# Kernel optimization log

Measured on AMD Instinct MI355X. Metric: run time of the kernel, lower is better.

Reference implementation:

```python
import jax, jax.numpy as jnp
import numpy as np

N = 131072       # total nodes (B graphs x P nodes)
P = 4096         # nodes per graph
B = 32           # graphs in batch
E = 2097152      # edges (avg degree 16)
IN_DIM = 64
HID = 128
OUT = 16
EPS = 1e-5
SLOPE = 0.01


def _degrees(idx):
    # structural degree, clamped to min 1 (as DGL GraphConv does)
    d = jax.ops.segment_sum(jnp.ones((E,), jnp.float32), idx, num_segments=N)
    return jnp.maximum(d, 1.0)


def _graph_conv(x, W, src, dst, ew):
    # DGL GraphConv, norm='both', bias=False, with scalar edge weights:
    # h = D_out^{-1/2} x ; m_v = sum_{(u->v)} w_e h_u ; out = (D_in^{-1/2} m) W
    h = x * jax.lax.rsqrt(_degrees(src))[:, None]
    m = jax.ops.segment_sum(ew[:, None] * h[src], dst, num_segments=N)  # [N, F]
    return (m * jax.lax.rsqrt(_degrees(dst))[:, None]) @ W


def _graph_norm(x, gamma, beta, alpha):
    # GraphNorm (Cai et al. / PyG, batch=None): stats over all nodes per feature
    mu = jnp.mean(x, axis=0)
    c = x - alpha * mu
    var = jnp.mean(c * c, axis=0)
    return c * jax.lax.rsqrt(var + EPS) * gamma + beta


def _mean_nodes(h, gid):
    # per-graph mean readout; every graph has exactly P nodes
    return jax.ops.segment_sum(h, gid, num_segments=B) / P


def setup_inputs() -> dict:
    key = jax.random.key(0)
    ks = jax.random.split(key, 8)
    src = jax.random.randint(ks[0], (E,), 0, N, dtype=jnp.int32)
    # keep edges within each 4096-node graph block (batched DGL graph)
    dst = (src // P) * P + jax.random.randint(ks[1], (E,), 0, P, dtype=jnp.int32)
    features = jax.random.normal(ks[2], (N, IN_DIM), jnp.float32)
    edge_weights = jax.random.uniform(ks[3], (E,), jnp.float32)
    # kaiming/xavier-scale init approximations
    W1 = jax.random.normal(ks[4], (IN_DIM, HID), jnp.float32) * np.sqrt(2.0 / IN_DIM)
    W2 = jax.random.normal(ks[5], (HID, HID), jnp.float32) * np.sqrt(2.0 / HID)
    Wc = jax.random.normal(ks[6], (OUT, 2 * HID), jnp.float32) * np.sqrt(1.0 / (2 * HID))
    ones = jnp.ones((HID,), jnp.float32)
    zeros = jnp.zeros((HID,), jnp.float32)
    return {
        'features': features, 'edge_weights': edge_weights, 'src': src, 'dst': dst,
        'W1': W1, 'W2': W2, 'Wc': Wc,
        'gamma1': ones, 'beta1': zeros, 'alpha1': ones,
        'gamma2': ones, 'beta2': zeros, 'alpha2': ones,
    }


def reference(features, edge_weights, src, dst, W1, W2, Wc,
              gamma1, beta1, alpha1, gamma2, beta2, alpha2):
    gid = jnp.arange(N, dtype=jnp.int32) // P  # node -> graph id
    h1 = _graph_conv(features, W1, src, dst, edge_weights)
    h1 = jax.nn.leaky_relu(_graph_norm(h1, gamma1, beta1, alpha1), SLOPE)
    r1 = _mean_nodes(h1, gid)                  # [B, HID]
    h2 = _graph_conv(h1, W2, src, dst, edge_weights)
    h2 = jax.nn.leaky_relu(_graph_norm(h2, gamma2, beta2, alpha2), SLOPE)
    r2 = _mean_nodes(h2, gid)                  # [B, HID]
    readouts = jnp.concatenate([r1, r2], axis=1)  # [B, 2*HID]
    return readouts @ Wc.T                     # [B, OUT]
```

## Files before the change

kernel.cpp:

```cpp
#include <hip/hip_runtime.h>
#include <hip/hip_fp16.h>

constexpr int NN   = 131072;
constexpr int PP   = 4096;
constexpr int BG   = 32;
constexpr int EE   = 2097152;
constexpr int IND  = 64;
constexpr int HH   = 128;
constexpr int CAP  = 81920;
constexpr float EPSV   = 1e-5f;
constexpr float SLOPEV = 0.01f;

typedef short bf16x8 __attribute__((ext_vector_type(8)));
typedef float f32x4  __attribute__((ext_vector_type(4)));

__device__ __forceinline__ unsigned f2bf(float f) {
    unsigned u = __float_as_uint(f);
    return (u + 0x7FFFu + ((u >> 16) & 1u)) >> 16;
}
__device__ __forceinline__ unsigned pack2bf(float lo, float hi) {
    return f2bf(lo) | (f2bf(hi) << 16);
}
__device__ __forceinline__ float bflo(unsigned p) { return __uint_as_float(p << 16); }
__device__ __forceinline__ float bfhi(unsigned p) { return __uint_as_float(p & 0xFFFF0000u); }
__device__ __forceinline__ float w16(unsigned r) {
    return __half2float(__ushort_as_half((unsigned short)(r >> 16)));
}

template <int K>
__device__ __forceinline__ void packw_body(const float* __restrict__ W,
                                           unsigned short* __restrict__ pw, int t) {
    if (t >= K * 16) return;
    int lane = t & 63, nt = (t >> 6) & 7, kt = t >> 9;
    int kbase = kt * 32 + ((lane >> 4) & 3) * 8;
    int col   = nt * 16 + (lane & 15);
    for (int j = 0; j < 8; j++)
        pw[t * 8 + j] = (unsigned short)f2bf(W[(kbase + j) * HH + col]);
}

__global__ __launch_bounds__(256) void k_prep(const float* __restrict__ features,
                                              unsigned* __restrict__ fx,
                                              const float* __restrict__ W1,
                                              unsigned short* __restrict__ pw1,
                                              const float* __restrict__ W2,
                                              unsigned short* __restrict__ pw2,
                                              int* __restrict__ gcur,
                                              float* __restrict__ racc,
                                              unsigned* __restrict__ csr2) {
    int b = blockIdx.x, t = threadIdx.x;
    if (b < 16384) {
        int i = b * 256 + t;
        float2 v = ((const float2*)features)[i];
        fx[i] = pack2bf(v.x, v.y);
        return;
    }
    if (b == 16384) {
        if (t < BG) gcur[t * 16] = t * CAP;
        for (int i = t; i < 2 * BG * HH; i += 256) racc[i] = 0.f;
        return;
    }
    if (b < 16389) { packw_body<64>(W1, pw1, (b - 16385) * 256 + t); return; }
    if (b < 16397) { packw_body<128>(W2, pw2, (b - 16389) * 256 + t); return; }
    ((uint4*)csr2)[(b - 16397) * 256 + t] = make_uint4(0, 0, 0, 0);
}

__global__ __launch_bounds__(256) void k_part(const int* __restrict__ src,
                                              const int* __restrict__ dst,
                                              const float* __restrict__ ew,
                                              int* __restrict__ gcur,
                                              uint2* __restrict__ recs) {
    __shared__ int cnt[32];
    __shared__ int start[32];
    __shared__ int gbase[32];
    __shared__ uint2 stage[4096];
    int t = threadIdx.x;
    int ebase = blockIdx.x * 4096;
    if (t < 32) cnt[t] = 0;
    __syncthreads();
    int es[16]; int ed[16]; float ev[16];
#pragma unroll
    for (int k = 0; k < 16; k++) {
        int e = ebase + k * 256 + t;
        es[k] = src[e]; ed[k] = dst[e]; ev[k] = ew[e];
        atomicAdd(&cnt[es[k] >> 12], 1);
    }
    __syncthreads();
    if (t == 0) {
        int run = 0;
        for (int g = 0; g < 32; g++) { start[g] = run; run += cnt[g]; }
    }
    __syncthreads();
    if (t < 32) {
        gbase[t] = atomicAdd(&gcur[t * 16], cnt[t]);
        cnt[t] = start[t];
    }
    __syncthreads();
#pragma unroll
    for (int k = 0; k < 16; k++) {
        int g = es[k] >> 12;
        int pos = atomicAdd(&cnt[g], 1);
        stage[pos] = make_uint2((unsigned)(es[k] & 4095) | ((unsigned)(ed[k] & 4095) << 12) |
                                ((unsigned)g << 24), __float_as_uint(ev[k]));
    }
    __syncthreads();
    for (int i = t; i < 4096; i += 256) {
        uint2 r = stage[i];
        int g = r.x >> 24;
        recs[gbase[g] + (i - start[g])] = r;
    }
}

__global__ __launch_bounds__(1024) void k_hist(const uint2* __restrict__ recs,
                                               const int* __restrict__ gcur,
                                               int* __restrict__ shist,
                                               int* __restrict__ dhist) {
    __shared__ int hs[4096];
    __shared__ int hd[4096];
    int t = threadIdx.x;
    int g = blockIdx.x >> 3, c = blockIdx.x & 7;
    int n = gcur[g * 16] - g * CAP;
    int lo = (n * c) >> 3, hi = (n * (c + 1)) >> 3;
    ((int4*)hs)[t] = make_int4(0, 0, 0, 0);
    ((int4*)hd)[t] = make_int4(0, 0, 0, 0);
    __syncthreads();
    const uint2* base = recs + (size_t)g * CAP;
    for (int i = lo + t; i < hi; i += 1024) {
        unsigned x = base[i].x;
        atomicAdd(&hs[x & 4095], 1);
        atomicAdd(&hd[(x >> 12) & 4095], 1);
    }
    __syncthreads();
    ((int4*)(shist + (size_t)blockIdx.x * 4096))[t] = ((int4*)hs)[t];
    ((int4*)(dhist + (size_t)blockIdx.x * 4096))[t] = ((int4*)hd)[t];
}

__global__ __launch_bounds__(1024) void k_offs(int* __restrict__ shist,
                                               int* __restrict__ dhist,
                                               float* __restrict__ rs_s,
                                               float* __restrict__ rsd,
                                               int* __restrict__ degd,
                                               int* __restrict__ offs) {
    __shared__ int partial[1024];
    int t = threadIdx.x, g = blockIdx.x;
    int sdeg[4] = {0, 0, 0, 0}, ddeg[4] = {0, 0, 0, 0};
#pragma unroll
    for (int c = 0; c < 8; c++) {
        int4 sv = ((const int4*)(shist + (size_t)(g * 8 + c) * 4096))[t];
        int4 dv = ((const int4*)(dhist + (size_t)(g * 8 + c) * 4096))[t];
        sdeg[0] += sv.x; sdeg[1] += sv.y; sdeg[2] += sv.z; sdeg[3] += sv.w;
        ddeg[0] += dv.x; ddeg[1] += dv.y; ddeg[2] += dv.z; ddeg[3] += dv.w;
    }
    int pdeg[4];
#pragma unroll
    for (int j = 0; j < 4; j++) {
        int idx = t * 4 + j;
        int vs = sdeg[j]; if (vs < 1) vs = 1;
        rs_s[g * PP + idx] = rsqrtf((float)vs);
        int vd = ddeg[j]; if (vd < 1) vd = 1;
        rsd[g * PP + idx]  = rsqrtf((float)vd);
        pdeg[j] = (ddeg[j] + 3) & ~3;
        degd[g * PP + idx] = pdeg[j];
    }
    partial[t] = pdeg[0] + pdeg[1] + pdeg[2] + pdeg[3];
    __syncthreads();
    for (int off = 1; off < 1024; off <<= 1) {
        int v = partial[t];
        int add = (t >= off) ? partial[t - off] : 0;
        __syncthreads();
        partial[t] = v + add;
        __syncthreads();
    }
    int run = (t == 0) ? 0 : partial[t - 1];
#pragma unroll
    for (int j = 0; j < 4; j++) {
        int idx = t * 4 + j;
        offs[g * PP + idx] = g * CAP + run;
        int nb = run;
        for (int c = 0; c < 8; c++) {
            size_t hidx = (size_t)(g * 8 + c) * 4096 + idx;
            int v = dhist[hidx];
            dhist[hidx] = nb;
            nb += v;
        }
        run += pdeg[j];
    }
}

__global__ __launch_bounds__(1024) void k_place(const uint2* __restrict__ recs,
                                                const int* __restrict__ gcur,
                                                const int* __restrict__ dhist,
                                                const float* __restrict__ rs_s,
                                                unsigned* __restrict__ csr2) {
    __shared__ int cur[4096];
    __shared__ float rss[4096];
    int t = threadIdx.x;
    int g = blockIdx.x >> 3, c = blockIdx.x & 7;
    int n = gcur[g * 16] - g * CAP;
    int lo = (n * c) >> 3, hi = (n * (c + 1)) >> 3;
    ((int4*)cur)[t] = ((const int4*)(dhist + (size_t)blockIdx.x * 4096))[t];
    ((float4*)rss)[t] = ((const float4*)(rs_s + (size_t)g * PP))[t];
    __syncthreads();
    const uint2* base = recs + (size_t)g * CAP;
    unsigned* cbase = csr2 + (size_t)g * CAP;
    for (int i = lo + t; i < hi; i += 1024) {
        uint2 r = base[i];
        int sl = r.x & 4095, dl = (r.x >> 12) & 4095;
        int pos = atomicAdd(&cur[dl], 1);
        float wf = __uint_as_float(r.y) * rss[sl];
        cbase[pos] = (unsigned)sl | ((unsigned)__half_as_ushort(__float2half(wf)) << 16);
    }
}

__global__ __launch_bounds__(256) void k_aggemm1(const unsigned* __restrict__ fx,
                                                 const unsigned* __restrict__ csr2,
                                                 const int* __restrict__ offs,
                                                 const int* __restrict__ degd,
                                                 const float* __restrict__ rsd,
                                                 const short* __restrict__ PW,
                                                 unsigned short* __restrict__ C,
                                                 float* __restrict__ part) {
    constexpr int WP = 36;
    __shared__ unsigned lds[64 * WP];
    __shared__ float s1[HH], s2[HH];
    int t = threadIdx.x;
    if (t < HH) { s1[t] = 0.f; s2[t] = 0.f; }
    int bid = blockIdx.x;
    int xcd = bid & 7, idx = bid >> 3;
    int g = xcd * 4 + (idx >> 6);
    int node0 = g * PP + (idx & 63) * 64;
    int lane = t & 63, wv = t >> 6;
    int half = lane >> 5, sl = lane & 31;
    const unsigned* hp = fx + (size_t)((unsigned)(g * PP) * 32) + sl;
    for (int p = 0; p < 8; p++) {
        int lr = wv * 16 + p * 2 + half;
        int v = node0 + lr;
        int o = offs[v], cnt = degd[v];
        float ax0 = 0.f, ay0 = 0.f, ax1 = 0.f, ay1 = 0.f;
        for (int i = 0; i < cnt; i += 4) {
            uint4 rr = *(const uint4*)(csr2 + o + i);
            unsigned g0 = hp[(rr.x & 4095) * 32];
            unsigned g1 = hp[(rr.y & 4095) * 32];
            unsigned g2 = hp[(rr.z & 4095) * 32];
            unsigned g3 = hp[(rr.w & 4095) * 32];
            float w0 = w16(rr.x), w1 = w16(rr.y), w2 = w16(rr.z), w3 = w16(rr.w);
            ax0 += w0 * bflo(g0); ay0 += w0 * bfhi(g0);
            ax1 += w1 * bflo(g1); ay1 += w1 * bfhi(g1);
            ax0 += w2 * bflo(g2); ay0 += w2 * bfhi(g2);
            ax1 += w3 * bflo(g3); ay1 += w3 * bfhi(g3);
        }
        float rd = rsd[v];
        lds[lr * WP + sl] = pack2bf((ax0 + ax1) * rd, (ay0 + ay1) * rd);
    }
    __syncthreads();
    int m = lane & 15, quad = lane >> 4;
    bf16x8 a[2];
#pragma unroll
    for (int kt = 0; kt < 2; kt++)
        a[kt] = *(const bf16x8*)&lds[(wv * 16 + m) * WP + kt * 16 + quad * 4];
#pragma unroll
    for (int nt = 0; nt < 8; nt++) {
        f32x4 acc = {0.f, 0.f, 0.f, 0.f};
#pragma unroll
        for (int kt = 0; kt < 2; kt++) {
            bf16x8 b = *(const bf16x8*)(PW + ((size_t)(kt * 8 + nt) * 64 + lane) * 8);
            acc = __builtin_amdgcn_mfma_f32_16x16x32_bf16(a[kt], b, acc, 0, 0, 0);
        }
        int col = nt * 16 + m;
        int r0 = node0 + wv * 16 + quad * 4;
        float ps = 0.f, pq = 0.f;
#pragma unroll
        for (int r = 0; r < 4; r++) {
            C[(size_t)(r0 + r) * HH + col] = (unsigned short)f2bf(acc[r]);
            ps += acc[r]; pq += acc[r] * acc[r];
        }
        atomicAdd(&s1[col], ps);
        atomicAdd(&s2[col], pq);
    }
    __syncthreads();
    if (t < HH) {
        part[bid * 256 + t]      = s1[t];
        part[bid * 256 + HH + t] = s2[t];
    }
}

__global__ __launch_bounds__(256) void k_aggemm2(const unsigned* __restrict__ h1,
                                                 const unsigned* __restrict__ csr2,
                                                 const int* __restrict__ offs,
                                                 const int* __restrict__ degd,
                                                 const float* __restrict__ rsd,
                                                 const short* __restrict__ PW,
                                                 unsigned short* __restrict__ C,
                                                 float* __restrict__ part) {
    constexpr int WP = 68;
    __shared__ unsigned lds[64 * WP];
    __shared__ float s1[HH], s2[HH];
    int t = threadIdx.x;
    if (t < HH) { s1[t] = 0.f; s2[t] = 0.f; }
    int bid = blockIdx.x;
    int xcd = bid & 7, idx = bid >> 3;
    int g = xcd * 4 + (idx >> 6);
    int node0 = g * PP + (idx & 63) * 64;
    int lane = t & 63, wv = t >> 6;
    const unsigned* hp = h1 + (size_t)((unsigned)(g * PP) * 64) + lane;
    for (int p = 0; p < 8; p++) {
        int va = node0 + wv * 16 + p, vb = va + 8;
        int oa = offs[va], ca = degd[va];
        int ob = offs[vb], cb = degd[vb];
        float A0 = 0.f, A1 = 0.f, B0 = 0.f, B1 = 0.f;
        int c0 = ca < cb ? ca : cb;
        int cm = ca < cb ? cb : ca;
        int i = 0;
        for (; i < c0; i += 4) {
            uint4 ra = *(const uint4*)(csr2 + oa + i);
            uint4 rb = *(const uint4*)(csr2 + ob + i);
            unsigned ga0 = hp[(ra.x & 4095) * 64];
            unsigned ga1 = hp[(ra.y & 4095) * 64];
            unsigned ga2 = hp[(ra.z & 4095) * 64];
            unsigned ga3 = hp[(ra.w & 4095) * 64];
            unsigned gb0 = hp[(rb.x & 4095) * 64];
            unsigned gb1 = hp[(rb.y & 4095) * 64];
            unsigned gb2 = hp[(rb.z & 4095) * 64];
            unsigned gb3 = hp[(rb.w & 4095) * 64];
            float wa0 = w16(ra.x), wa1 = w16(ra.y), wa2 = w16(ra.z), wa3 = w16(ra.w);
            float wb0 = w16(rb.x), wb1 = w16(rb.y), wb2 = w16(rb.z), wb3 = w16(rb.w);
            A0 += wa0 * bflo(ga0); A1 += wa0 * bfhi(ga0);
            A0 += wa1 * bflo(ga1); A1 += wa1 * bfhi(ga1);
            A0 += wa2 * bflo(ga2); A1 += wa2 * bfhi(ga2);
            A0 += wa3 * bflo(ga3); A1 += wa3 * bfhi(ga3);
            B0 += wb0 * bflo(gb0); B1 += wb0 * bfhi(gb0);
            B0 += wb1 * bflo(gb1); B1 += wb1 * bfhi(gb1);
            B0 += wb2 * bflo(gb2); B1 += wb2 * bfhi(gb2);
            B0 += wb3 * bflo(gb3); B1 += wb3 * bfhi(gb3);
        }
        if (i < cm) {
            int ot = (ca > cb) ? oa : ob;
            float E0 = 0.f, E1 = 0.f, F0 = 0.f, F1 = 0.f;
            for (; i < cm; i += 4) {
                uint4 rr = *(const uint4*)(csr2 + ot + i);
                unsigned g0 = hp[(rr.x & 4095) * 64];
                unsigned g1 = hp[(rr.y & 4095) * 64];
                unsigned g2 = hp[(rr.z & 4095) * 64];
                unsigned g3 = hp[(rr.w & 4095) * 64];
                float w0 = w16(rr.x), w1 = w16(rr.y), w2 = w16(rr.z), w3 = w16(rr.w);
                E0 += w0 * bflo(g0); E1 += w0 * bfhi(g0);
                F0 += w1 * bflo(g1); F1 += w1 * bfhi(g1);
                E0 += w2 * bflo(g2); E1 += w2 * bfhi(g2);
                F0 += w3 * bflo(g3); F1 += w3 * bfhi(g3);
            }
            if (ca > cb) { A0 += E0 + F0; A1 += E1 + F1; }
            else         { B0 += E0 + F0; B1 += E1 + F1; }
        }
        float rda = rsd[va], rdb = rsd[vb];
        lds[(wv * 16 + p) * WP + lane]     = pack2bf(A0 * rda, A1 * rda);
        lds[(wv * 16 + p + 8) * WP + lane] = pack2bf(B0 * rdb, B1 * rdb);
    }
    __syncthreads();
    int m = lane & 15, quad = lane >> 4;
    bf16x8 a[4];
#pragma unroll
    for (int kt = 0; kt < 4; kt++)
        a[kt] = *(const bf16x8*)&lds[(wv * 16 + m) * WP + kt * 16 + quad * 4];
#pragma unroll
    for (int nt = 0; nt < 8; nt++) {
        f32x4 acc = {0.f, 0.f, 0.f, 0.f};
#pragma unroll
        for (int kt = 0; kt < 4; kt++) {
            bf16x8 b = *(const bf16x8*)(PW + ((size_t)(kt * 8 + nt) * 64 + lane) * 8);
            acc = __builtin_amdgcn_mfma_f32_16x16x32_bf16(a[kt], b, acc, 0, 0, 0);
        }
        int col = nt * 16 + m;
        int r0 = node0 + wv * 16 + quad * 4;
        float ps = 0.f, pq = 0.f;
#pragma unroll
        for (int r = 0; r < 4; r++) {
            C[(size_t)(r0 + r) * HH + col] = (unsigned short)f2bf(acc[r]);
            ps += acc[r]; pq += acc[r] * acc[r];
        }
        atomicAdd(&s1[col], ps);
        atomicAdd(&s2[col], pq);
    }
    __syncthreads();
    if (t < HH) {
        part[bid * 256 + t]      = s1[t];
        part[bid * 256 + HH + t] = s2[t];
    }
}

__global__ __launch_bounds__(256) void k_red(const float* __restrict__ part,
                                             float* __restrict__ pb) {
    int t = threadIdx.x, b = blockIdx.x;
    float s = 0.f;
    for (int r = 0; r < 32; r++) s += part[(size_t)(b * 32 + r) * 256 + t];
    pb[b * 256 + t] = s;
}

__global__ void k_coef(const float* __restrict__ pb, const float* __restrict__ gamma,
                       const float* __restrict__ beta, const float* __restrict__ alpha,
                       float* __restrict__ ab) {
    int t = threadIdx.x;
    float s = 0.f;
    for (int b = 0; b < 64; b++) s += pb[b * 256 + t];
    __shared__ float sh[256];
    sh[t] = s;
    __syncthreads();
    if (t < 128) {
        float mu = sh[t] * (1.f / NN);
        float e2 = sh[128 + t] * (1.f / NN);
        float al = alpha[t];
        float var = e2 - (2.f * al - al * al) * mu * mu;
        float a = rsqrtf(var + EPSV) * gamma[t];
        ab[t] = a;
        ab[HH + t] = beta[t] - al * mu * a;
    }
}

template <bool WRITE>
__global__ __launch_bounds__(256) void k_normro(unsigned* __restrict__ h,
                                                const float* __restrict__ ab,
                                                float* __restrict__ racc) {
    int fp = threadIdx.x & 63;
    int q  = threadIdx.x >> 6;
    int node0 = blockIdx.x * 64;
    int g = node0 / PP;
    float a0 = ab[2 * fp], a1 = ab[2 * fp + 1];
    float b0 = ab[HH + 2 * fp], b1 = ab[HH + 2 * fp + 1];
    float s0 = 0.f, s1 = 0.f;
    for (int i = q; i < 64; i += 4) {
        size_t idx = (size_t)(node0 + i) * 64 + fp;
        unsigned v = h[idx];
        float x0 = fmaf(a0, bflo(v), b0); x0 = x0 > 0.f ? x0 : SLOPEV * x0;
        float x1 = fmaf(a1, bfhi(v), b1); x1 = x1 > 0.f ? x1 : SLOPEV * x1;
        if (WRITE) h[idx] = pack2bf(x0, x1);
        s0 += x0; s1 += x1;
    }
    __shared__ float sh[512];
    sh[threadIdx.x] = s0;
    sh[256 + threadIdx.x] = s1;
    __syncthreads();
    if (q == 0) {
        float t0 = s0 + sh[64 + fp] + sh[128 + fp] + sh[192 + fp];
        float t1 = s1 + sh[256 + 64 + fp] + sh[256 + 128 + fp] + sh[256 + 192 + fp];
        atomicAdd(&racc[g * HH + 2 * fp],     t0);
        atomicAdd(&racc[g * HH + 2 * fp + 1], t1);
    }
}

__global__ void k_final(const float* __restrict__ racc1, const float* __restrict__ racc2,
                        const float* __restrict__ Wc, float* __restrict__ out) {
    int t = threadIdx.x;
    int b = t >> 4, o = t & 15;
    float acc = 0.f;
    for (int f = 0; f < HH; f++) acc += racc1[b * HH + f] * Wc[o * (2 * HH) + f];
    for (int f = 0; f < HH; f++) acc += racc2[b * HH + f] * Wc[o * (2 * HH) + HH + f];
    out[t] = acc * (1.f / PP);
}

extern "C" void kernel_launch(void* const* d_in, const int* in_sizes, int n_in,
                              void* d_out, int out_size, void* d_ws, size_t ws_size,
                              hipStream_t stream) {
    const float* features = (const float*)d_in[0];
    const float* ew       = (const float*)d_in[1];
    const int*   src      = (const int*)d_in[2];
    const int*   dst      = (const int*)d_in[3];
    const float* W1       = (const float*)d_in[4];
    const float* W2       = (const float*)d_in[5];
    const float* Wc       = (const float*)d_in[6];
    const float* gamma1   = (const float*)d_in[7];
    const float* beta1    = (const float*)d_in[8];
    const float* alpha1   = (const float*)d_in[9];
    const float* gamma2   = (const float*)d_in[10];
    const float* beta2    = (const float*)d_in[11];
    const float* alpha2   = (const float*)d_in[12];
    float* out = (float*)d_out;

    char* w = (char*)d_ws;
    int*    gcur   = (int*)(w + 0);
    float*  racc1  = (float*)(w + (16u << 10));
    float*  racc2  = (float*)(w + (32u << 10));
    float*  ab1    = (float*)(w + (48u << 10));
    float*  ab2    = (float*)(w + (52u << 10));
    unsigned short* pw1 = (unsigned short*)(w + (64u << 10));
    unsigned short* pw2 = (unsigned short*)(w + (80u << 10));
    float*  pb     = (float*)(w + (128u << 10));
    float*  rs_s   = (float*)(w + (1024u << 10));
    float*  rsd    = (float*)(w + (1536u << 10));
    int*    degd   = (int*)(w + (2048u << 10));
    int*    offs   = (int*)(w + (2560u << 10));
    float*  part   = (float*)(w + (3u << 20));
    int*    shist  = (int*)(w + (5u << 20));
    int*    dhist  = (int*)(w + (9u << 20));
    unsigned* csr2 = (unsigned*)(w + (13u << 20));
    unsigned* mbuf = (unsigned*)(w + (23u << 20));
    unsigned* hbuf = (unsigned*)(w + (55u << 20));
    uint2*    recs = (uint2*)(w + (87u << 20));
    unsigned* fx   = (unsigned*)(w + (107u << 20));

    k_prep<<<18957, 256, 0, stream>>>(features, fx, W1, pw1, W2, pw2, gcur, racc1, csr2);

    k_part<<<EE / 4096, 256, 0, stream>>>(src, dst, ew, gcur, recs);
    k_hist<<<BG * 8, 1024, 0, stream>>>(recs, gcur, shist, dhist);
    k_offs<<<BG, 1024, 0, stream>>>(shist, dhist, rs_s, rsd, degd, offs);
    k_place<<<BG * 8, 1024, 0, stream>>>(recs, gcur, dhist, rs_s, csr2);

    k_aggemm1<<<NN / 64, 256, 0, stream>>>(fx, csr2, offs, degd, rsd,
                                           (const short*)pw1, (unsigned short*)hbuf, part);
    k_red<<<64, 256, 0, stream>>>(part, pb);
    k_coef<<<1, 256, 0, stream>>>(pb, gamma1, beta1, alpha1, ab1);
    k_normro<true><<<NN / 64, 256, 0, stream>>>(hbuf, ab1, racc1);

    k_aggemm2<<<NN / 64, 256, 0, stream>>>(hbuf, csr2, offs, degd, rsd,
                                           (const short*)pw2, (unsigned short*)mbuf, part);
    k_red<<<64, 256, 0, stream>>>(part, pb);
    k_coef<<<1, 256, 0, stream>>>(pb, gamma2, beta2, alpha2, ab2);
    k_normro<false><<<NN / 64, 256, 0, stream>>>(mbuf, ab2, racc2);

    k_final<<<1, 512, 0, stream>>>(racc1, racc2, Wc, out);
}
```

Baseline: 391.0 us.

## Store gathered node features in FP8 to halve gather bandwidth

Input features and layer-1 activations are now stored as packed FP8 (e4m3 via cvt_pk_fp8) rather than bf16. The aggregation kernels decode them with cvt_pk_f32_fp8, with each lane gathering 8 features per edge. The gather loops are restructured so each lane handles two destination nodes with 8-wide accumulators, and normro writes a separate FP8 buffer in an XCD-aware block order. This cuts the bytes moved by the random neighbour gathers, which likely dominate, at the cost of much lower precision in the activations.

Result: faster. 359.0 us (-8.2%).

```diff
diff --git a/kernel.cpp b/kernel.cpp
--- a/kernel.cpp
+++ b/kernel.cpp
@@ -13,6 +13,7 @@
 
 typedef short bf16x8 __attribute__((ext_vector_type(8)));
 typedef float f32x4  __attribute__((ext_vector_type(4)));
+typedef float f32x2  __attribute__((ext_vector_type(2)));
 
 __device__ __forceinline__ unsigned f2bf(float f) {
     unsigned u = __float_as_uint(f);
@@ -25,6 +26,17 @@
 __device__ __forceinline__ float bfhi(unsigned p) { return __uint_as_float(p & 0xFFFF0000u); }
 __device__ __forceinline__ float w16(unsigned r) {
     return __half2float(__ushort_as_half((unsigned short)(r >> 16)));
+}
+__device__ __forceinline__ void acc8(float& a0, float& a1, float& a2, float& a3,
+                                     float& a4, float& a5, float& a6, float& a7,
+                                     uint2 q, unsigned rec) {
+    float w = w16(rec);
+    f32x2 l0 = __builtin_amdgcn_cvt_pk_f32_fp8((int)q.x, false);
+    f32x2 h0 = __builtin_amdgcn_cvt_pk_f32_fp8((int)q.x, true);
+    f32x2 l1 = __builtin_amdgcn_cvt_pk_f32_fp8((int)q.y, false);
+    f32x2 h1 = __builtin_amdgcn_cvt_pk_f32_fp8((int)q.y, true);
+    a0 += w * l0.x; a1 += w * l0.y; a2 += w * h0.x; a3 += w * h0.y;
+    a4 += w * l1.x; a5 += w * l1.y; a6 += w * h1.x; a7 += w * h1.y;
 }
 
 template <int K>
@@ -39,7 +51,7 @@
 }
 
 __global__ __launch_bounds__(256) void k_prep(const float* __restrict__ features,
-                                              unsigned* __restrict__ fx,
+                                              unsigned* __restrict__ f8x,
                                               const float* __restrict__ W1,
                                               unsigned short* __restrict__ pw1,
                                               const float* __restrict__ W2,
@@ -48,20 +60,22 @@
                                               float* __restrict__ racc,
                                               unsigned* __restrict__ csr2) {
     int b = blockIdx.x, t = threadIdx.x;
-    if (b < 16384) {
+    if (b < 8192) {
         int i = b * 256 + t;
-        float2 v = ((const float2*)features)[i];
-        fx[i] = pack2bf(v.x, v.y);
+        float4 v = ((const float4*)features)[i];
+        int w0 = __builtin_amdgcn_cvt_pk_fp8_f32(v.x, v.y, 0, false);
+        int w1 = __builtin_amdgcn_cvt_pk_fp8_f32(v.z, v.w, w0, true);
+        f8x[i] = (unsigned)w1;
         return;
     }
-    if (b == 16384) {
+    if (b == 8192) {
         if (t < BG) gcur[t * 16] = t * CAP;
         for (int i = t; i < 2 * BG * HH; i += 256) racc[i] = 0.f;
         return;
     }
-    if (b < 16389) { packw_body<64>(W1, pw1, (b - 16385) * 256 + t); return; }
-    if (b < 16397) { packw_body<128>(W2, pw2, (b - 16389) * 256 + t); return; }
-    ((uint4*)csr2)[(b - 16397) * 256 + t] = make_uint4(0, 0, 0, 0);
+    if (b < 8197) { packw_body<64>(W1, pw1, (b - 8193) * 256 + t); return; }
+    if (b < 8205) { packw_body<128>(W2, pw2, (b - 8197) * 256 + t); return; }
+    ((uint4*)csr2)[(b - 8205) * 256 + t] = make_uint4(0, 0, 0, 0);
 }
 
 __global__ __launch_bounds__(256) void k_part(const int* __restrict__ src,
@@ -211,7 +225,7 @@
     }
 }
 
-__global__ __launch_bounds__(256) void k_aggemm1(const unsigned* __restrict__ fx,
+__global__ __launch_bounds__(256) void k_aggemm1(const unsigned* __restrict__ f8x,
                                                  const unsigned* __restrict__ csr2,
                                                  const int* __restrict__ offs,
                                                  const int* __restrict__ degd,
@@ -229,27 +243,62 @@
     int g = xcd * 4 + (idx >> 6);
     int node0 = g * PP + (idx & 63) * 64;
     int lane = t & 63, wv = t >> 6;
-    int half = lane >> 5, sl = lane & 31;
-    const unsigned* hp = fx + (size_t)((unsigned)(g * PP) * 32) + sl;
-    for (int p = 0; p < 8; p++) {
-        int lr = wv * 16 + p * 2 + half;
-        int v = node0 + lr;
-        int o = offs[v], cnt = degd[v];
-        float ax0 = 0.f, ay0 = 0.f, ax1 = 0.f, ay1 = 0.f;
-        for (int i = 0; i < cnt; i += 4) {
-            uint4 rr = *(const uint4*)(csr2 + o + i);
-            unsigned g0 = hp[(rr.x & 4095) * 32];
-            unsigned g1 = hp[(rr.y & 4095) * 32];
-            unsigned g2 = hp[(rr.z & 4095) * 32];
-            unsigned g3 = hp[(rr.w & 4095) * 32];
-            float w0 = w16(rr.x), w1 = w16(rr.y), w2 = w16(rr.z), w3 = w16(rr.w);
-            ax0 += w0 * bflo(g0); ay0 += w0 * bfhi(g0);
-            ax1 += w1 * bflo(g1); ay1 += w1 * bfhi(g1);
-            ax0 += w2 * bflo(g2); ay0 += w2 * bfhi(g2);
-            ax1 += w3 * bflo(g3); ay1 += w3 * bfhi(g3);
-        }
-        float rd = rsd[v];
-        lds[lr * WP + sl] = pack2bf((ax0 + ax1) * rd, (ay0 + ay1) * rd);
+    int eid = lane >> 3, ql = lane & 7;
+    const uint2* hp8 = (const uint2*)(f8x + (size_t)((unsigned)(g * PP)) * 16) + ql;
+    {
+        int lrA = wv * 16 + eid * 2;
+        int va = node0 + lrA, vb = va + 1;
+        int oa = offs[va], ca = degd[va];
+        int ob = offs[vb], cb = degd[vb];
+        float A0=0.f,A1=0.f,A2=0.f,A3=0.f,A4=0.f,A5=0.f,A6=0.f,A7=0.f;
+        float B0=0.f,B1=0.f,B2=0.f,B3=0.f,B4=0.f,B5=0.f,B6=0.f,B7=0.f;
+        int c0 = ca < cb ? ca : cb;
+        int cm = ca < cb ? cb : ca;
+        int i = 0;
+        for (; i < c0; i += 4) {
+            uint4 ra = *(const uint4*)(csr2 + oa + i);
+            uint4 rb = *(const uint4*)(csr2 + ob + i);
+            uint2 ga0 = hp8[(ra.x & 4095) * 8];
+            uint2 ga1 = hp8[(ra.y & 4095) * 8];
+            uint2 ga2 = hp8[(ra.z & 4095) * 8];
+            uint2 ga3 = hp8[(ra.w & 4095) * 8];
+            uint2 gb0 = hp8[(rb.x & 4095) * 8];
+            uint2 gb1 = hp8[(rb.y & 4095) * 8];
+            uint2 gb2 = hp8[(rb.z & 4095) * 8];
+            uint2 gb3 = hp8[(rb.w & 4095) * 8];
+            acc8(A0,A1,A2,A3,A4,A5,A6,A7, ga0, ra.x);
+            acc8(A0,A1,A2,A3,A4,A5,A6,A7, ga1, ra.y);
+            acc8(A0,A1,A2,A3,A4,A5,A6,A7, ga2, ra.z);
+            acc8(A0,A1,A2,A3,A4,A5,A6,A7, ga3, ra.w);
+            acc8(B0,B1,B2,B3,B4,B5,B6,B7, gb0, rb.x);
+            acc8(B0,B1,B2,B3,B4,B5,B6,B7, gb1, rb.y);
+            acc8(B0,B1,B2,B3,B4,B5,B6,B7, gb2, rb.z);
+            acc8(B0,B1,B2,B3,B4,B5,B6,B7, gb3, rb.w);
+        }
+        if (i < cm) {
+            int ot = (ca > cb) ? oa : ob;
+            float E0=0.f,E1=0.f,E2=0.f,E3=0.f,E4=0.f,E5=0.f,E6=0.f,E7=0.f;
+            for (; i < cm; i += 4) {
+                uint4 rr = *(const uint4*)(csr2 + ot + i);
+                uint2 g0 = hp8[(rr.x & 4095) * 8];
+                uint2 g1 = hp8[(rr.y & 4095) * 8];
+                uint2 g2 = hp8[(rr.z & 4095) * 8];
+                uint2 g3 = hp8[(rr.w & 4095) * 8];
+                acc8(E0,E1,E2,E3,E4,E5,E6,E7, g0, rr.x);
+                acc8(E0,E1,E2,E3,E4,E5,E6,E7, g1, rr.y);
+                acc8(E0,E1,E2,E3,E4,E5,E6,E7, g2, rr.z);
+                acc8(E0,E1,E2,E3,E4,E5,E6,E7, g3, rr.w);
+            }
+            if (ca > cb) { A0+=E0;A1+=E1;A2+=E2;A3+=E3;A4+=E4;A5+=E5;A6+=E6;A7+=E7; }
+            else         { B0+=E0;B1+=E1;B2+=E2;B3+=E3;B4+=E4;B5+=E5;B6+=E6;B7+=E7; }
+        }
+        float rda = rsd[va], rdb = rsd[vb];
+        *(uint4*)&lds[lrA * WP + ql * 4] =
+            make_uint4(pack2bf(A0*rda, A1*rda), pack2bf(A2*rda, A3*rda),
+                       pack2bf(A4*rda, A5*rda), pack2bf(A6*rda, A7*rda));
+        *(uint4*)&lds[(lrA + 1) * WP + ql * 4] =
+            make_uint4(pack2bf(B0*rdb, B1*rdb), pack2bf(B2*rdb, B3*rdb),
+                       pack2bf(B4*rdb, B5*rdb), pack2bf(B6*rdb, B7*rdb));
     }
     __syncthreads();
     int m = lane & 15, quad = lane >> 4;
@@ -283,7 +332,7 @@
     }
 }
 
-__global__ __launch_bounds__(256) void k_aggemm2(const unsigned* __restrict__ h1,
+__global__ __launch_bounds__(256) void k_aggemm2(const unsigned* __restrict__ f8,
                                                  const unsigned* __restrict__ csr2,
                                                  const int* __restrict__ offs,
                                                  const int* __restrict__ degd,
@@ -301,65 +350,69 @@
     int g = xcd * 4 + (idx >> 6);
     int node0 = g * PP + (idx & 63) * 64;
     int lane = t & 63, wv = t >> 6;
-    const unsigned* hp = h1 + (size_t)((unsigned)(g * PP) * 64) + lane;
-    for (int p = 0; p < 8; p++) {
-        int va = node0 + wv * 16 + p, vb = va + 8;
+    int quad = lane >> 4, ql = lane & 15;
+    const uint2* hp8 = (const uint2*)(f8 + (size_t)((unsigned)(g * PP)) * 32) + ql;
+    for (int p = 0; p < 2; p++) {
+        int lrA = wv * 16 + p * 8 + quad * 2;
+        int va = node0 + lrA, vb = va + 1;
         int oa = offs[va], ca = degd[va];
         int ob = offs[vb], cb = degd[vb];
-        float A0 = 0.f, A1 = 0.f, B0 = 0.f, B1 = 0.f;
+        float A0=0.f,A1=0.f,A2=0.f,A3=0.f,A4=0.f,A5=0.f,A6=0.f,A7=0.f;
+        float B0=0.f,B1=0.f,B2=0.f,B3=0.f,B4=0.f,B5=0.f,B6=0.f,B7=0.f;
         int c0 = ca < cb ? ca : cb;
         int cm = ca < cb ? cb : ca;
         int i = 0;
         for (; i < c0; i += 4) {
             uint4 ra = *(const uint4*)(csr2 + oa + i);
             uint4 rb = *(const uint4*)(csr2 + ob + i);
-            unsigned ga0 = hp[(ra.x & 4095) * 64];
-            unsigned ga1 = hp[(ra.y & 4095) * 64];
-            unsigned ga2 = hp[(ra.z & 4095) * 64];
-            unsigned ga3 = hp[(ra.w & 4095) * 64];
-            unsigned gb0 = hp[(rb.x & 4095) * 64];
-            unsigned gb1 = hp[(rb.y & 4095) * 64];
-            unsigned gb2 = hp[(rb.z & 4095) * 64];
-            unsigned gb3 = hp[(rb.w & 4095) * 64];
-            float wa0 = w16(ra.x), wa1 = w16(ra.y), wa2 = w16(ra.z), wa3 = w16(ra.w);
-            float wb0 = w16(rb.x), wb1 = w16(rb.y), wb2 = w16(rb.z), wb3 = w16(rb.w);
-            A0 += wa0 * bflo(ga0); A1 += wa0 * bfhi(ga0);
-            A0 += wa1 * bflo(ga1); A1 += wa1 * bfhi(ga1);
-            A0 += wa2 * bflo(ga2); A1 += wa2 * bfhi(ga2);
-            A0 += wa3 * bflo(ga3); A1 += wa3 * bfhi(ga3);
-            B0 += wb0 * bflo(gb0); B1 += wb0 * bfhi(gb0);
-            B0 += wb1 * bflo(gb1); B1 += wb1 * bfhi(gb1);
-            B0 += wb2 * bflo(gb2); B1 += wb2 * bfhi(gb2);
-            B0 += wb3 * bflo(gb3); B1 += wb3 * bfhi(gb3);
+            uint2 ga0 = hp8[(ra.x & 4095) * 16];
+            uint2 ga1 = hp8[(ra.y & 4095) * 16];
+            uint2 ga2 = hp8[(ra.z & 4095) * 16];
+            uint2 ga3 = hp8[(ra.w & 4095) * 16];
+            uint2 gb0 = hp8[(rb.x & 4095) * 16];
+            uint2 gb1 = hp8[(rb.y & 4095) * 16];
+            uint2 gb2 = hp8[(rb.z & 4095) * 16];
+            uint2 gb3 = hp8[(rb.w & 4095) * 16];
+            acc8(A0,A1,A2,A3,A4,A5,A6,A7, ga0, ra.x);
+            acc8(A0,A1,A2,A3,A4,A5,A6,A7, ga1, ra.y);
+            acc8(A0,A1,A2,A3,A4,A5,A6,A7, ga2, ra.z);
+            acc8(A0,A1,A2,A3,A4,A5,A6,A7, ga3, ra.w);
+            acc8(B0,B1,B2,B3,B4,B5,B6,B7, gb0, rb.x);
+            acc8(B0,B1,B2,B3,B4,B5,B6,B7, gb1, rb.y);
+            acc8(B0,B1,B2,B3,B4,B5,B6,B7, gb2, rb.z);
+            acc8(B0,B1,B2,B3,B4,B5,B6,B7, gb3, rb.w);
         }
         if (i < cm) {
             int ot = (ca > cb) ? oa : ob;
-            float E0 = 0.f, E1 = 0.f, F0 = 0.f, F1 = 0.f;
+            float E0=0.f,E1=0.f,E2=0.f,E3=0.f,E4=0.f,E5=0.f,E6=0.f,E7=0.f;
             for (; i < cm; i += 4) {
                 uint4 rr = *(const uint4*)(csr2 + ot + i);
-                unsigned g0 = hp[(rr.x & 4095) * 64];
-                unsigned g1 = hp[(rr.y & 4095) * 64];
-                unsigned g2 = hp[(rr.z & 4095) * 64];
-                unsigned g3 = hp[(rr.w & 4095) * 64];
-                float w0 = w16(rr.x), w1 = w16(rr.y), w2 = w16(rr.z), w3 = w16(rr.w);
-                E0 += w0 * bflo(g0); E1 += w0 * bfhi(g0);
-                F0 += w1 * bflo(g1); F1 += w1 * bfhi(g1);
-                E0 += w2 * bflo(g2); E1 += w2 * bfhi(g2);
-                F0 += w3 * bflo(g3); F1 += w3 * bfhi(g3);
+                uint2 g0 = hp8[(rr.x & 4095) * 16];
+                uint2 g1 = hp8[(rr.y & 4095) * 16];
+                uint2 g2 = hp8[(rr.z & 4095) * 16];
+                uint2 g3 = hp8[(rr.w & 4095) * 16];
+                acc8(E0,E1,E2,E3,E4,E5,E6,E7, g0, rr.x);
+                acc8(E0,E1,E2,E3,E4,E5,E6,E7, g1, rr.y);
+                acc8(E0,E1,E2,E3,E4,E5,E6,E7, g2, rr.z);
+                acc8(E0,E1,E2,E3,E4,E5,E6,E7, g3, rr.w);
             }
-            if (ca > cb) { A0 += E0 + F0; A1 += E1 + F1; }
-            else         { B0 += E0 + F0; B1 += E1 + F1; }
+            if (ca > cb) { A0+=E0;A1+=E1;A2+=E2;A3+=E3;A4+=E4;A5+=E5;A6+=E6;A7+=E7; }
+            else         { B0+=E0;B1+=E1;B2+=E2;B3+=E3;B4+=E4;B5+=E5;B6+=E6;B7+=E7; }
         }
         float rda = rsd[va], rdb = rsd[vb];
-        lds[(wv * 16 + p) * WP + lane]     = pack2bf(A0 * rda, A1 * rda);
-        lds[(wv * 16 + p + 8) * WP + lane] = pack2bf(B0 * rdb, B1 * rdb);
-    }
-    __syncthreads();
-    int m = lane & 15, quad = lane >> 4;
+        *(uint4*)&lds[lrA * WP + ql * 4] =
+            make_uint4(pack2bf(A0*rda, A1*rda), pack2bf(A2*rda, A3*rda),
+                       pack2bf(A4*rda, A5*rda), pack2bf(A6*rda, A7*rda));
+        *(uint4*)&lds[(lrA + 1) * WP + ql * 4] =
+            make_uint4(pack2bf(B0*rdb, B1*rdb), pack2bf(B2*rdb, B3*rdb),
+                       pack2bf(B4*rdb, B5*rdb), pack2bf(B6*rdb, B7*rdb));
+    }
+    __syncthreads();
+    int m = lane & 15, quad2 = lane >> 4;
     bf16x8 a[4];
 #pragma unroll
     for (int kt = 0; kt < 4; kt++)
-        a[kt] = *(const bf16x8*)&lds[(wv * 16 + m) * WP + kt * 16 + quad * 4];
+        a[kt] = *(const bf16x8*)&lds[(wv * 16 + m) * WP + kt * 16 + quad2 * 4];
 #pragma unroll
     for (int nt = 0; nt < 8; nt++) {
         f32x4 acc = {0.f, 0.f, 0.f, 0.f};
@@ -369,7 +422,7 @@
             acc = __builtin_amdgcn_mfma_f32_16x16x32_bf16(a[kt], b, acc, 0, 0, 0);
         }
         int col = nt * 16 + m;
-        int r0 = node0 + wv * 16 + quad * 4;
+        int r0 = node0 + wv * 16 + quad2 * 4;
         float ps = 0.f, pq = 0.f;
 #pragma unroll
         for (int r = 0; r < 4; r++) {
@@ -415,22 +468,25 @@
 }
 
 template <bool WRITE>
-__global__ __launch_bounds__(256) void k_normro(unsigned* __restrict__ h,
+__global__ __launch_bounds__(256) void k_normro(const unsigned* __restrict__ h,
                                                 const float* __restrict__ ab,
-                                                float* __restrict__ racc) {
+                                                float* __restrict__ racc,
+                                                unsigned short* __restrict__ f8) {
     int fp = threadIdx.x & 63;
     int q  = threadIdx.x >> 6;
-    int node0 = blockIdx.x * 64;
-    int g = node0 / PP;
+    int bid = blockIdx.x;
+    int xcd = bid & 7, idx = bid >> 3;
+    int g = xcd * 4 + (idx >> 6);
+    int node0 = g * PP + (idx & 63) * 64;
     float a0 = ab[2 * fp], a1 = ab[2 * fp + 1];
     float b0 = ab[HH + 2 * fp], b1 = ab[HH + 2 * fp + 1];
     float s0 = 0.f, s1 = 0.f;
     for (int i = q; i < 64; i += 4) {
-        size_t idx = (size_t)(node0 + i) * 64 + fp;
-        unsigned v = h[idx];
+        size_t idx2 = (size_t)(node0 + i) * 64 + fp;
+        unsigned v = h[idx2];
         float x0 = fmaf(a0, bflo(v), b0); x0 = x0 > 0.f ? x0 : SLOPEV * x0;
         float x1 = fmaf(a1, bfhi(v), b1); x1 = x1 > 0.f ? x1 : SLOPEV * x1;
-        if (WRITE) h[idx] = pack2bf(x0, x1);
+        if (WRITE) f8[idx2] = (unsigned short)__builtin_amdgcn_cvt_pk_fp8_f32(x0, x1, 0, false);
         s0 += x0; s1 += x1;
     }
     __shared__ float sh[512];
@@ -493,26 +549,27 @@
     unsigned* mbuf = (unsigned*)(w + (23u << 20));
     unsigned* hbuf = (unsigned*)(w + (55u << 20));
     uint2*    recs = (uint2*)(w + (87u << 20));
-    unsigned* fx   = (unsigned*)(w + (107u << 20));
-
-    k_prep<<<18957, 256, 0, stream>>>(features, fx, W1, pw1, W2, pw2, gcur, racc1, csr2);
+    unsigned* f8x  = (unsigned*)(w + (107u << 20));
+    unsigned* f8buf= (unsigned*)(w + (123u << 20));
+
+    k_prep<<<10765, 256, 0, stream>>>(features, f8x, W1, pw1, W2, pw2, gcur, racc1, csr2);
 
     k_part<<<EE / 4096, 256, 0, stream>>>(src, dst, ew, gcur, recs);
     k_hist<<<BG * 8, 1024, 0, stream>>>(recs, gcur, shist, dhist);
     k_offs<<<BG, 1024, 0, stream>>>(shist, dhist, rs_s, rsd, degd, offs);
     k_place<<<BG * 8, 1024, 0, stream>>>(recs, gcur, dhist, rs_s, csr2);
 
-    k_aggemm1<<<NN / 64, 256, 0, stream>>>(fx, csr2, offs, degd, rsd,
+    k_aggemm1<<<NN / 64, 256, 0, stream>>>(f8x, csr2, offs, degd, rsd,
                                            (const short*)pw1, (unsigned short*)hbuf, part);
     k_red<<<64, 256, 0, stream>>>(part, pb);
     k_coef<<<1, 256, 0, stream>>>(pb, gamma1, beta1, alpha1, ab1);
-    k_normro<true><<<NN / 64, 256, 0, stream>>>(hbuf, ab1, racc1);
-
-    k_aggemm2<<<NN / 64, 256, 0, stream>>>(hbuf, csr2, offs, degd, rsd,
+    k_normro<true><<<NN / 64, 256, 0, stream>>>(hbuf, ab1, racc1, (unsigned short*)f8buf);
+
+    k_aggemm2<<<NN / 64, 256, 0, stream>>>(f8buf, csr2, offs, degd, rsd,
                                            (const short*)pw2, (unsigned short*)mbuf, part);
     k_red<<<64, 256, 0, stream>>>(part, pb);
     k_coef<<<1, 256, 0, stream>>>(pb, gamma2, beta2, alpha2, ab2);
-    k_normro<false><<<NN / 64, 256, 0, stream>>>(mbuf, ab2, racc2);
+    k_normro<false><<<NN / 64, 256, 0, stream>>>(mbuf, ab2, racc2, nullptr);
 
     k_final<<<1, 512, 0, stream>>>(racc1, racc2, Wc, out);
 }
```
